# Kernel tuning notes

Measured on AMD Instinct MI355X. Metric: run time of the kernel, lower is better.

Reference implementation:

```python
import jax, jax.numpy as jnp
import numpy as np
from jax import lax

C_RED = 32
IN_CH = 256
BN_EPS = 1e-5
NORM_EPS = 1e-6


def setup_inputs() -> dict:
    key = jax.random.key(0)
    ks = jax.random.split(key, 5)
    B, H, W = 16, 64, 64
    x = jax.random.normal(ks[0], (B, IN_CH, H, W), dtype=jnp.float32)
    w_reduce = jax.random.normal(ks[1], (C_RED, IN_CH), dtype=jnp.float32) * 0.05
    bn_gamma = jnp.ones((C_RED,), dtype=jnp.float32)
    bn_beta = jnp.zeros((C_RED,), dtype=jnp.float32)
    bn_mean = jax.random.normal(ks[2], (C_RED,), dtype=jnp.float32) * 0.1
    bn_var = jax.random.uniform(ks[3], (C_RED,), dtype=jnp.float32, minval=0.5, maxval=1.5)
    # depthwise 3x3 kernel, OIHW with I=1 (groups == channels)
    dw_weight = jax.random.normal(ks[4], (C_RED, 1, 3, 3), dtype=jnp.float32) * 0.1
    scale = jnp.ones((C_RED,), dtype=jnp.float32)
    return {"x": x, "w_reduce": w_reduce, "bn_gamma": bn_gamma, "bn_beta": bn_beta,
            "bn_mean": bn_mean, "bn_var": bn_var, "dw_weight": dw_weight, "scale": scale}


def _l2_normalize(t):
    # F.normalize(p=2, dim=1, eps=1e-6): divide by max(||t||_2, eps) along channel dim
    n = jnp.sqrt(jnp.sum(t * t, axis=1, keepdims=True))
    return t / jnp.maximum(n, NORM_EPS)


def reference(x, w_reduce, bn_gamma, bn_beta, bn_mean, bn_var, dw_weight, scale):
    # 1x1 reduce conv (no bias)
    z = jnp.einsum('bihw,oi->bohw', x, w_reduce)
    # BatchNorm2d (inference: running stats)
    inv = bn_gamma / jnp.sqrt(bn_var + BN_EPS)
    z = z * inv[None, :, None, None] + (bn_beta - bn_mean * inv)[None, :, None, None]
    z = jax.nn.relu(z)
    # SpiralTwist: depthwise 3x3 conv (SAME) then per-channel scale
    z_tw = lax.conv_general_dilated(
        z, dw_weight, window_strides=(1, 1), padding='SAME',
        feature_group_count=C_RED,
        dimension_numbers=('NCHW', 'OIHW', 'NCHW'))
    z_tw = z_tw * scale[None, :, None, None]
    z_norm = _l2_normalize(z)
    z_tw_norm = _l2_normalize(z_tw)
    # upper-triangular channel pairs (i <= j)
    idx_i, idx_j = np.triu_indices(C_RED, k=0)
    pair = z_norm[:, idx_i] * z_tw_norm[:, idx_j]  # [B, C*(C+1)/2, H, W]
    return jnp.concatenate([z_norm, pair], axis=1)
```

## Files before the change

### kernel.cpp

```cpp
#include <hip/hip_runtime.h>
#include <hip/hip_bf16.h>
#include <stdint.h>

#define HW   4096
#define CIN  256
#define CR   32
#define COUT 560

__global__ __launch_bounds__(256) void k_conv1x1(
    const float* __restrict__ x,
    const float* __restrict__ wr,
    const float* __restrict__ gamma,
    const float* __restrict__ beta,
    const float* __restrict__ mean,
    const float* __restrict__ var,
    float* __restrict__ z)
{
    const int tid = threadIdx.x;
    const int og  = __builtin_amdgcn_readfirstlane(tid >> 6);
    const int g0  = blockIdx.x * 64 + (tid & 63);
    const int b   = g0 >> 12;
    const int p   = g0 & 4095;

    const float* xb = x + ((((size_t)b) * CIN) << 12) + p;
    const float* wp = wr + (size_t)og * 8 * CIN;

    float acc[8] = {0.f,0.f,0.f,0.f,0.f,0.f,0.f,0.f};

    for (int cc = 0; cc < 16; ++cc) {
        float xv[16];
        #pragma unroll
        for (int k = 0; k < 16; ++k)
            xv[k] = xb[((size_t)(cc * 16 + k)) << 12];
        #pragma unroll
        for (int o = 0; o < 8; ++o) {
            #pragma unroll
            for (int k = 0; k < 16; ++k)
                acc[o] = fmaf(xv[k], wp[o * CIN + cc * 16 + k], acc[o]);
        }
    }

    #pragma unroll
    for (int o = 0; o < 8; ++o) {
        const int oc = og * 8 + o;
        const float inv = gamma[oc] / sqrtf(var[oc] + 1e-5f);
        const float bia = beta[oc] - mean[oc] * inv;
        z[((((size_t)b) * CR + oc) << 12) + p] =
            fmaxf(fmaf(acc[o], inv, bia), 0.f);
    }
}

__global__ __launch_bounds__(256) void k_twist(
    const float* __restrict__ z,
    const float* __restrict__ dww,
    const float* __restrict__ scl,
    float* __restrict__ out)
{
    __shared__ float dml[CR * 9];
    __shared__ float sc[CR];
    __shared__ float ps1[4 * 64];
    __shared__ float ps2[4 * 64];
    __shared__ float znl[CR * 64];
    __shared__ float twl[CR * 64];

    const int tid = threadIdx.x;
    for (int t = tid; t < CR * 9; t += 256) dml[t] = dww[t];
    if (tid < CR) sc[tid] = scl[tid];
    __syncthreads();

    const int cg  = __builtin_amdgcn_readfirstlane(tid >> 6);
    const int px  = tid & 63;
    const int g0  = blockIdx.x * 64;
    const int b   = g0 >> 12;
    const int p0  = g0 & 4095;
    const int h   = p0 >> 6;
    const float* zb = z + (((size_t)b * CR) << 12);

    float zc[8], tw[8];
    float s1 = 0.f, s2 = 0.f;
    #pragma unroll
    for (int k = 0; k < 8; ++k) {
        const int c = cg * 8 + k;
        const float* zp = zb + ((size_t)c << 12);
        float acc = 0.f, center = 0.f;
        #pragma unroll
        for (int dy = 0; dy < 3; ++dy) {
            const int hy = h + dy - 1;
            const bool rok = ((unsigned)hy) < 64u;
            #pragma unroll
            for (int dx = 0; dx < 3; ++dx) {
                const int wx = px + dx - 1;
                const bool ok = rok && (((unsigned)wx) < 64u);
                float v = 0.f;
                if (ok) v = zp[(hy << 6) + wx];
                if (dy == 1 && dx == 1) center = v;
                acc = fmaf(v, dml[c * 9 + dy * 3 + dx], acc);
            }
        }
        const float t = acc * sc[c];
        zc[k] = center; tw[k] = t;
        s1 = fmaf(center, center, s1);
        s2 = fmaf(t, t, s2);
    }
    ps1[cg * 64 + px] = s1;
    ps2[cg * 64 + px] = s2;
    __syncthreads();
    const float t1 = ps1[px] + ps1[64 + px] + ps1[128 + px] + ps1[192 + px];
    const float t2 = ps2[px] + ps2[64 + px] + ps2[128 + px] + ps2[192 + px];
    const float rn1 = 1.0f / fmaxf(sqrtf(t1), 1e-6f);
    const float rn2 = 1.0f / fmaxf(sqrtf(t2), 1e-6f);
    #pragma unroll
    for (int k = 0; k < 8; ++k) {
        znl[(cg * 8 + k) * 64 + px] = zc[k] * rn1;
        twl[(cg * 8 + k) * 64 + px] = tw[k] * rn2;
    }
    __syncthreads();

    float* outb = out + (((size_t)b * COUT) << 12) + p0 + px;
    #pragma unroll
    for (int P = 0; P < 32; ++P)
        if ((P & 3) == cg)
            outb[(size_t)P << 12] = znl[P * 64 + px];
    {
        int P = 32;
        #pragma unroll
        for (int i = 0; i < CR; ++i) {
            #pragma unroll
            for (int j = i; j < CR; ++j) {
                if ((P & 3) == cg)
                    outb[(size_t)P << 12] = znl[i * 64 + px] * twl[j * 64 + px];
                ++P;
            }
        }
    }
}

extern "C" void kernel_launch(void* const* d_in, const int* in_sizes, int n_in,
                              void* d_out, int out_size, void* d_ws, size_t ws_size,
                              hipStream_t stream) {
    const float* x     = (const float*)d_in[0];
    const float* wr    = (const float*)d_in[1];
    const float* gamma = (const float*)d_in[2];
    const float* beta  = (const float*)d_in[3];
    const float* mean  = (const float*)d_in[4];
    const float* var   = (const float*)d_in[5];
    const float* dww   = (const float*)d_in[6];
    const float* scl   = (const float*)d_in[7];
    float* z = (float*)d_ws;
    float* out = (float*)d_out;

    hipLaunchKernelGGL(k_conv1x1, dim3(1024), dim3(256), 0, stream,
                       x, wr, gamma, beta, mean, var, z);
    hipLaunchKernelGGL(k_twist, dim3(1024), dim3(256), 0, stream,
                       z, dww, scl, out);
}
```

Before: 240.1 us.

## Vectorize both kernels with float4 pixels and restructure pair output loop

Both kernels now process four adjacent pixels per thread with float4 loads and stores. The 1x1 conv uses 512-thread blocks with 4 output channels per wave instead of 8. The twist kernel tiles 4 rows per block and computes the 3x3 stencil from float4 neighbours. The pair-product stage drops the predicated full triangular loop: each wave owns channels j and writes only its pairs, with the twist values kept in registers. The aim is fewer memory instructions and less wasted predicated work on a store-bound output. The cost is a 4x smaller grid (256 blocks), which may reduce occupancy across the CUs.

After: 225.1 us. 6.3% less time.

```diff
diff --git a/kernel.cpp b/kernel.cpp
--- a/kernel.cpp
+++ b/kernel.cpp
@@ -1,13 +1,11 @@
 #include <hip/hip_runtime.h>
-#include <hip/hip_bf16.h>
 #include <stdint.h>
 
-#define HW   4096
 #define CIN  256
 #define CR   32
 #define COUT 560
 
-__global__ __launch_bounds__(256) void k_conv1x1(
+__global__ __launch_bounds__(512) void k_conv1x1(
     const float* __restrict__ x,
     const float* __restrict__ wr,
     const float* __restrict__ gamma,
@@ -18,35 +16,64 @@
 {
     const int tid = threadIdx.x;
     const int og  = __builtin_amdgcn_readfirstlane(tid >> 6);
-    const int g0  = blockIdx.x * 64 + (tid & 63);
-    const int b   = g0 >> 12;
-    const int p   = g0 & 4095;
-
-    const float* xb = x + ((((size_t)b) * CIN) << 12) + p;
-    const float* wp = wr + (size_t)og * 8 * CIN;
-
-    float acc[8] = {0.f,0.f,0.f,0.f,0.f,0.f,0.f,0.f};
-
+    const int q   = tid & 63;
+    const int blk = blockIdx.x;
+    const int b   = blk >> 4;
+    const int p0  = (blk & 15) << 8;
+
+    const float* xb = x + ((((size_t)b) * CIN) << 12) + p0 + (q << 2);
+    const float* wp = wr + og * 4 * CIN;
+
+    float4 a0 = {0.f,0.f,0.f,0.f};
+    float4 a1 = {0.f,0.f,0.f,0.f};
+    float4 a2 = {0.f,0.f,0.f,0.f};
+    float4 a3 = {0.f,0.f,0.f,0.f};
+
+    #pragma unroll 2
     for (int cc = 0; cc < 16; ++cc) {
-        float xv[16];
+        float4 xv[16];
         #pragma unroll
         for (int k = 0; k < 16; ++k)
-            xv[k] = xb[((size_t)(cc * 16 + k)) << 12];
+            xv[k] = *(const float4*)(xb + ((size_t)(cc * 16 + k) << 12));
         #pragma unroll
-        for (int o = 0; o < 8; ++o) {
-            #pragma unroll
-            for (int k = 0; k < 16; ++k)
-                acc[o] = fmaf(xv[k], wp[o * CIN + cc * 16 + k], acc[o]);
+        for (int k = 0; k < 16; ++k) {
+            const int ic = cc * 16 + k;
+            const float w0 = wp[           ic];
+            const float w1 = wp[    CIN  + ic];
+            const float w2 = wp[2 * CIN  + ic];
+            const float w3 = wp[3 * CIN  + ic];
+            a0.x = fmaf(xv[k].x, w0, a0.x);
+            a0.y = fmaf(xv[k].y, w0, a0.y);
+            a0.z = fmaf(xv[k].z, w0, a0.z);
+            a0.w = fmaf(xv[k].w, w0, a0.w);
+            a1.x = fmaf(xv[k].x, w1, a1.x);
+            a1.y = fmaf(xv[k].y, w1, a1.y);
+            a1.z = fmaf(xv[k].z, w1, a1.z);
+            a1.w = fmaf(xv[k].w, w1, a1.w);
+            a2.x = fmaf(xv[k].x, w2, a2.x);
+            a2.y = fmaf(xv[k].y, w2, a2.y);
+            a2.z = fmaf(xv[k].z, w2, a2.z);
+            a2.w = fmaf(xv[k].w, w2, a2.w);
+            a3.x = fmaf(xv[k].x, w3, a3.x);
+            a3.y = fmaf(xv[k].y, w3, a3.y);
+            a3.z = fmaf(xv[k].z, w3, a3.z);
+            a3.w = fmaf(xv[k].w, w3, a3.w);
         }
     }
 
-    #pragma unroll
-    for (int o = 0; o < 8; ++o) {
-        const int oc = og * 8 + o;
+    float4* zq = (float4*)(z + (((size_t)b * CR) << 12) + p0 + (q << 2));
+    #pragma unroll
+    for (int o = 0; o < 4; ++o) {
+        const int oc = og * 4 + o;
         const float inv = gamma[oc] / sqrtf(var[oc] + 1e-5f);
         const float bia = beta[oc] - mean[oc] * inv;
-        z[((((size_t)b) * CR + oc) << 12) + p] =
-            fmaxf(fmaf(acc[o], inv, bia), 0.f);
+        const float4 a = (o == 0) ? a0 : (o == 1) ? a1 : (o == 2) ? a2 : a3;
+        float4 r;
+        r.x = fmaxf(fmaf(a.x, inv, bia), 0.f);
+        r.y = fmaxf(fmaf(a.y, inv, bia), 0.f);
+        r.z = fmaxf(fmaf(a.z, inv, bia), 0.f);
+        r.w = fmaxf(fmaf(a.w, inv, bia), 0.f);
+        zq[(size_t)oc << 10] = r;
     }
 }
 
@@ -56,81 +83,116 @@
     const float* __restrict__ scl,
     float* __restrict__ out)
 {
-    __shared__ float dml[CR * 9];
-    __shared__ float sc[CR];
-    __shared__ float ps1[4 * 64];
-    __shared__ float ps2[4 * 64];
-    __shared__ float znl[CR * 64];
-    __shared__ float twl[CR * 64];
-
-    const int tid = threadIdx.x;
-    for (int t = tid; t < CR * 9; t += 256) dml[t] = dww[t];
-    if (tid < CR) sc[tid] = scl[tid];
-    __syncthreads();
-
-    const int cg  = __builtin_amdgcn_readfirstlane(tid >> 6);
-    const int px  = tid & 63;
-    const int g0  = blockIdx.x * 64;
-    const int b   = g0 >> 12;
-    const int p0  = g0 & 4095;
-    const int h   = p0 >> 6;
+    __shared__ float4 znl4[CR][64];
+    __shared__ float4 ps1[4][64];
+    __shared__ float4 ps2[4][64];
+
+    const int tid  = threadIdx.x;
+    const int cg   = __builtin_amdgcn_readfirstlane(tid >> 6);
+    const int lane = tid & 63;
+    const int r    = lane >> 4;
+    const int cq   = lane & 15;
+    const int blk  = blockIdx.x;
+    const int b    = blk >> 4;
+    const int h0   = (blk & 15) << 2;
+    const int hh   = h0 + r;
+
     const float* zb = z + (((size_t)b * CR) << 12);
 
-    float zc[8], tw[8];
-    float s1 = 0.f, s2 = 0.f;
+    float4 zc[8], tw[8];
+    float4 s1 = {0.f,0.f,0.f,0.f};
+    float4 s2 = {0.f,0.f,0.f,0.f};
+
     #pragma unroll
     for (int k = 0; k < 8; ++k) {
-        const int c = cg * 8 + k;
+        const int c = cg + 4 * k;
         const float* zp = zb + ((size_t)c << 12);
-        float acc = 0.f, center = 0.f;
+        float4 acc = {0.f,0.f,0.f,0.f};
+        float4 ctr = {0.f,0.f,0.f,0.f};
         #pragma unroll
         for (int dy = 0; dy < 3; ++dy) {
-            const int hy = h + dy - 1;
+            const int hy = hh + dy - 1;
             const bool rok = ((unsigned)hy) < 64u;
-            #pragma unroll
-            for (int dx = 0; dx < 3; ++dx) {
-                const int wx = px + dx - 1;
-                const bool ok = rok && (((unsigned)wx) < 64u);
-                float v = 0.f;
-                if (ok) v = zp[(hy << 6) + wx];
-                if (dy == 1 && dx == 1) center = v;
-                acc = fmaf(v, dml[c * 9 + dy * 3 + dx], acc);
+            const float* zr = zp + (hy << 6);
+            float4 M  = {0.f,0.f,0.f,0.f};
+            float4 L4 = {0.f,0.f,0.f,0.f};
+            float4 R4 = {0.f,0.f,0.f,0.f};
+            if (rok) {
+                M = *(const float4*)(zr + (cq << 2));
+                if (cq > 0)  L4 = *(const float4*)(zr + (cq << 2) - 4);
+                if (cq < 15) R4 = *(const float4*)(zr + (cq << 2) + 4);
             }
+            const float w0 = dww[c * 9 + dy * 3 + 0];
+            const float w1 = dww[c * 9 + dy * 3 + 1];
+            const float w2 = dww[c * 9 + dy * 3 + 2];
+            acc.x = fmaf(w0, L4.w, fmaf(w1, M.x, fmaf(w2, M.y, acc.x)));
+            acc.y = fmaf(w0, M.x,  fmaf(w1, M.y, fmaf(w2, M.z, acc.y)));
+            acc.z = fmaf(w0, M.y,  fmaf(w1, M.z, fmaf(w2, M.w, acc.z)));
+            acc.w = fmaf(w0, M.z,  fmaf(w1, M.w, fmaf(w2, R4.x, acc.w)));
+            if (dy == 1) ctr = M;
         }
-        const float t = acc * sc[c];
-        zc[k] = center; tw[k] = t;
-        s1 = fmaf(center, center, s1);
-        s2 = fmaf(t, t, s2);
-    }
-    ps1[cg * 64 + px] = s1;
-    ps2[cg * 64 + px] = s2;
+        const float s = scl[c];
+        float4 t;
+        t.x = acc.x * s;  t.y = acc.y * s;  t.z = acc.z * s;  t.w = acc.w * s;
+        zc[k] = ctr;  tw[k] = t;
+        s1.x = fmaf(ctr.x, ctr.x, s1.x);  s1.y = fmaf(ctr.y, ctr.y, s1.y);
+        s1.z = fmaf(ctr.z, ctr.z, s1.z);  s1.w = fmaf(ctr.w, ctr.w, s1.w);
+        s2.x = fmaf(t.x, t.x, s2.x);      s2.y = fmaf(t.y, t.y, s2.y);
+        s2.z = fmaf(t.z, t.z, s2.z);      s2.w = fmaf(t.w, t.w, s2.w);
+    }
+
+    ps1[cg][lane] = s1;
+    ps2[cg][lane] = s2;
     __syncthreads();
-    const float t1 = ps1[px] + ps1[64 + px] + ps1[128 + px] + ps1[192 + px];
-    const float t2 = ps2[px] + ps2[64 + px] + ps2[128 + px] + ps2[192 + px];
-    const float rn1 = 1.0f / fmaxf(sqrtf(t1), 1e-6f);
-    const float rn2 = 1.0f / fmaxf(sqrtf(t2), 1e-6f);
+
+    float4 t1, t2;
+    {
+        const float4 u0 = ps1[0][lane], u1 = ps1[1][lane],
+                     u2 = ps1[2][lane], u3 = ps1[3][lane];
+        t1.x = u0.x + u1.x + u2.x + u3.x;  t1.y = u0.y + u1.y + u2.y + u3.y;
+        t1.z = u0.z + u1.z + u2.z + u3.z;  t1.w = u0.w + u1.w + u2.w + u3.w;
+        const float4 v0 = ps2[0][lane], v1 = ps2[1][lane],
+                     v2 = ps2[2][lane], v3 = ps2[3][lane];
+        t2.x = v0.x + v1.x + v2.x + v3.x;  t2.y = v0.y + v1.y + v2.y + v3.y;
+        t2.z = v0.z + v1.z + v2.z + v3.z;  t2.w = v0.w + v1.w + v2.w + v3.w;
+    }
+    float4 rn1, rn2;
+    rn1.x = 1.0f / fmaxf(sqrtf(t1.x), 1e-6f);
+    rn1.y = 1.0f / fmaxf(sqrtf(t1.y), 1e-6f);
+    rn1.z = 1.0f / fmaxf(sqrtf(t1.z), 1e-6f);
+    rn1.w = 1.0f / fmaxf(sqrtf(t1.w), 1e-6f);
+    rn2.x = 1.0f / fmaxf(sqrtf(t2.x), 1e-6f);
+    rn2.y = 1.0f / fmaxf(sqrtf(t2.y), 1e-6f);
+    rn2.z = 1.0f / fmaxf(sqrtf(t2.z), 1e-6f);
+    rn2.w = 1.0f / fmaxf(sqrtf(t2.w), 1e-6f);
+
+    float4* outq = (float4*)(out + (((size_t)b * COUT) << 12) + (hh << 6)) + cq;
+
     #pragma unroll
     for (int k = 0; k < 8; ++k) {
-        znl[(cg * 8 + k) * 64 + px] = zc[k] * rn1;
-        twl[(cg * 8 + k) * 64 + px] = tw[k] * rn2;
+        const int c = cg + 4 * k;
+        float4 zn;
+        zn.x = zc[k].x * rn1.x;  zn.y = zc[k].y * rn1.y;
+        zn.z = zc[k].z * rn1.z;  zn.w = zc[k].w * rn1.w;
+        outq[(size_t)c << 10] = zn;
+        znl4[c][lane] = zn;
+        tw[k].x *= rn2.x;  tw[k].y *= rn2.y;
+        tw[k].z *= rn2.z;  tw[k].w *= rn2.w;
     }
     __syncthreads();
 
-    float* outb = out + (((size_t)b * COUT) << 12) + p0 + px;
-    #pragma unroll
-    for (int P = 0; P < 32; ++P)
-        if ((P & 3) == cg)
-            outb[(size_t)P << 12] = znl[P * 64 + px];
-    {
-        int P = 32;
-        #pragma unroll
-        for (int i = 0; i < CR; ++i) {
-            #pragma unroll
-            for (int j = i; j < CR; ++j) {
-                if ((P & 3) == cg)
-                    outb[(size_t)P << 12] = znl[i * 64 + px] * twl[j * 64 + px];
-                ++P;
-            }
+    #pragma unroll
+    for (int k = 0; k < 8; ++k) {
+        const int j = cg + 4 * k;
+        const float4 t = tw[k];
+        int P = 32 + j;
+        for (int i = 0; i <= j; ++i) {
+            const float4 zi = znl4[i][lane];
+            float4 v;
+            v.x = zi.x * t.x;  v.y = zi.y * t.y;
+            v.z = zi.z * t.z;  v.w = zi.w * t.w;
+            outq[(size_t)P << 10] = v;
+            P += 31 - i;
         }
     }
 }
@@ -146,11 +208,11 @@
     const float* var   = (const float*)d_in[5];
     const float* dww   = (const float*)d_in[6];
     const float* scl   = (const float*)d_in[7];
-    float* z = (float*)d_ws;
+    float* z   = (float*)d_ws;
     float* out = (float*)d_out;
 
-    hipLaunchKernelGGL(k_conv1x1, dim3(1024), dim3(256), 0, stream,
+    hipLaunchKernelGGL(k_conv1x1, dim3(256), dim3(512), 0, stream,
                        x, wr, gamma, beta, mean, var, z);
-    hipLaunchKernelGGL(k_twist, dim3(1024), dim3(256), 0, stream,
+    hipLaunchKernelGGL(k_twist, dim3(256), dim3(256), 0, stream,
                        z, dww, scl, out);
 }
```
